# Performance work log

Measured on AMD Instinct MI355X. Metric: run time of the kernel, lower is better.

## Reference

```python
import jax, jax.numpy as jnp
import numpy as np

BS, DIM = 8192, 768
TEMPERATURE = 1.0
EPS = 1e-8


def setup_inputs() -> dict:
    key = jax.random.key(0)
    k1, k2 = jax.random.split(key)
    text_emb = jax.random.normal(k1, (BS, DIM), dtype=jnp.float32)
    ctr_emb = jax.random.normal(k2, (BS, DIM), dtype=jnp.float32)
    return {"text_emb": text_emb, "ctr_emb": ctr_emb}


def _l2norm(x):
    # cosine scorer normalization
    return x / jnp.maximum(jnp.linalg.norm(x, axis=-1, keepdims=True), EPS)


def reference(text_emb, ctr_emb):
    t = _l2norm(text_emb)          # [bs, d]
    c = _l2norm(ctr_emb)           # [bs, d]
    # S[i, j] = cos(text_i, ctr_j) / T  -- single GEMM instead of (bs,bs,d) broadcast
    S = jnp.einsum('id,jd->ij', t, c) / TEMPERATURE   # [bs, bs]
    sim_ii = jnp.diagonal(S)                           # [bs]
    # loss1_i = lse_j S[i,j] - S[i,i]; loss2_i = lse_j S[j,i] - S[i,i]
    loss = (jax.nn.logsumexp(S, axis=1)
            + jax.nn.logsumexp(S, axis=0)
            - 2.0 * sim_ii)
    return jnp.mean(loss)
```

## Files before the change

### kernel.cpp

```cpp
#include <hip/hip_runtime.h>
#include <hip/hip_bf16.h>

#define BS   8192
#define DIM  768
#define TILE 128
#define BK   128

typedef float f32x4 __attribute__((ext_vector_type(4)));
typedef int   i32x4 __attribute__((ext_vector_type(4)));
typedef int   i32x8 __attribute__((ext_vector_type(8)));

__device__ __forceinline__ void async16(const void* g, void* l) {
    __builtin_amdgcn_global_load_lds(
        (const __attribute__((address_space(1))) unsigned int*)g,
        (__attribute__((address_space(3))) unsigned int*)l,
        16, 0, 0);
}

__global__ __launch_bounds__(256) void normalize_kernel(
    const float* __restrict__ text, const float* __restrict__ ctr,
    unsigned char* __restrict__ tq, unsigned char* __restrict__ cq,
    float* __restrict__ sim) {
    const int lane = threadIdx.x & 63;
    const int row  = blockIdx.x * 4 + (threadIdx.x >> 6);
    const size_t base = (size_t)row * DIM;

    float4 t[3], c[3];
    float st = 0.f, sc = 0.f, sd = 0.f;
#pragma unroll
    for (int i = 0; i < 3; ++i) {
        t[i] = *(const float4*)&text[base + lane * 4 + i * 256];
        c[i] = *(const float4*)&ctr [base + lane * 4 + i * 256];
        st += t[i].x*t[i].x + t[i].y*t[i].y + t[i].z*t[i].z + t[i].w*t[i].w;
        sc += c[i].x*c[i].x + c[i].y*c[i].y + c[i].z*c[i].z + c[i].w*c[i].w;
        sd += t[i].x*c[i].x + t[i].y*c[i].y + t[i].z*c[i].z + t[i].w*c[i].w;
    }
#pragma unroll
    for (int off = 1; off < 64; off <<= 1) {
        st += __shfl_xor(st, off);
        sc += __shfl_xor(sc, off);
        sd += __shfl_xor(sd, off);
    }
    const float invt = 1.0f / fmaxf(sqrtf(st), 1e-8f);
    const float invc = 1.0f / fmaxf(sqrtf(sc), 1e-8f);
#pragma unroll
    for (int i = 0; i < 3; ++i) {
        unsigned int wt = (unsigned int)__builtin_amdgcn_cvt_pk_fp8_f32(t[i].x * invt, t[i].y * invt, 0, false);
        wt = (unsigned int)__builtin_amdgcn_cvt_pk_fp8_f32(t[i].z * invt, t[i].w * invt, (int)wt, true);
        unsigned int wcq = (unsigned int)__builtin_amdgcn_cvt_pk_fp8_f32(c[i].x * invc, c[i].y * invc, 0, false);
        wcq = (unsigned int)__builtin_amdgcn_cvt_pk_fp8_f32(c[i].z * invc, c[i].w * invc, (int)wcq, true);
        *(unsigned int*)&tq[base + lane * 4 + i * 256] = wt;
        *(unsigned int*)&cq[base + lane * 4 + i * 256] = wcq;
    }
    if (lane == 0) sim[row] = sd * invt * invc;
}

__global__ __launch_bounds__(256) void gemm_lse_kernel(
    const unsigned char* __restrict__ tq, const unsigned char* __restrict__ cq,
    float* __restrict__ rowsum, float* __restrict__ colsum) {
    __shared__ char ldsA[TILE * BK];
    __shared__ char ldsB[TILE * BK];

    const int tid = threadIdx.x;

    const int bid = blockIdx.x;
    const int xcd = bid & 7, idx = bid >> 3;
    const int tileCol = idx >> 3, rowInBand = idx & 7;
    const int rowBase = (xcd * 8 + rowInBand) * TILE;
    const int colBase = tileCol * TILE;

    const int wave = tid >> 6, lane = tid & 63;
    const int wr = wave >> 1, wc = wave & 1;
    const int quad = lane >> 4, l16 = lane & 15;

    int goff[4];
    char *dstA[4], *dstB[4];
#pragma unroll
    for (int i = 0; i < 4; ++i) {
        const int p  = tid + i * 256;
        const int kc = p >> 8;
        const int row = (p >> 1) & 127;
        const int hl  = (p & 1) ^ (kc & 1);
        goff[i] = row * DIM + kc * 32 + hl * 16;
        dstA[i] = ldsA + p * 16;
        dstB[i] = ldsB + p * 16;
    }
    const unsigned char* gA = tq + (size_t)rowBase * DIM;
    const unsigned char* gB = cq + (size_t)colBase * DIM;

    const int sw = quad & 1;
    int aoff[4], boff[4];
#pragma unroll
    for (int mt = 0; mt < 4; ++mt) aoff[mt] = quad * 4096 + (wr * 64 + mt * 16 + l16) * 32;
#pragma unroll
    for (int nt = 0; nt < 4; ++nt) boff[nt] = quad * 4096 + (wc * 64 + nt * 16 + l16) * 32;

    f32x4 acc[4][4];
#pragma unroll
    for (int mt = 0; mt < 4; ++mt)
#pragma unroll
        for (int nt = 0; nt < 4; ++nt)
            acc[mt][nt] = (f32x4){0.f, 0.f, 0.f, 0.f};

    for (int k0 = 0; k0 < DIM; k0 += BK) {
#pragma unroll
        for (int i = 0; i < 4; ++i) {
            async16(gA + goff[i] + k0, dstA[i]);
            async16(gB + goff[i] + k0, dstB[i]);
        }
        __syncthreads();

        i32x8 af[4], bf[4];
#pragma unroll
        for (int mt = 0; mt < 4; ++mt) {
            i32x4 lo = *(const i32x4*)(ldsA + aoff[mt] + sw * 16);
            i32x4 hi = *(const i32x4*)(ldsA + aoff[mt] + (sw ^ 1) * 16);
            af[mt] = __builtin_shufflevector(lo, hi, 0, 1, 2, 3, 4, 5, 6, 7);
        }
#pragma unroll
        for (int nt = 0; nt < 4; ++nt) {
            i32x4 lo = *(const i32x4*)(ldsB + boff[nt] + sw * 16);
            i32x4 hi = *(const i32x4*)(ldsB + boff[nt] + (sw ^ 1) * 16);
            bf[nt] = __builtin_shufflevector(lo, hi, 0, 1, 2, 3, 4, 5, 6, 7);
        }

#pragma unroll
        for (int mt = 0; mt < 4; ++mt)
#pragma unroll
            for (int nt = 0; nt < 4; ++nt)
                acc[mt][nt] = __builtin_amdgcn_mfma_scale_f32_16x16x128_f8f6f4(
                    af[mt], bf[nt], acc[mt][nt], 0, 0, 0, 127, 0, 127);
        __syncthreads();
    }

    float rp[4][4];
    float cp[4];
#pragma unroll
    for (int mt = 0; mt < 4; ++mt)
#pragma unroll
        for (int r = 0; r < 4; ++r) rp[mt][r] = 0.f;
#pragma unroll
    for (int nt = 0; nt < 4; ++nt) cp[nt] = 0.f;

#pragma unroll
    for (int mt = 0; mt < 4; ++mt)
#pragma unroll
        for (int nt = 0; nt < 4; ++nt)
#pragma unroll
            for (int r = 0; r < 4; ++r) {
                const float e = __expf(acc[mt][nt][r]);
                rp[mt][r] += e;
                cp[nt]    += e;
            }

#pragma unroll
    for (int mt = 0; mt < 4; ++mt)
#pragma unroll
        for (int r = 0; r < 4; ++r) {
            float v = rp[mt][r];
            v += __shfl_xor(v, 1);
            v += __shfl_xor(v, 2);
            v += __shfl_xor(v, 4);
            v += __shfl_xor(v, 8);
            rp[mt][r] = v;
        }
    if (l16 == 0) {
#pragma unroll
        for (int mt = 0; mt < 4; ++mt)
#pragma unroll
            for (int r = 0; r < 4; ++r)
                atomicAdd(&rowsum[rowBase + wr * 64 + mt * 16 + quad * 4 + r], rp[mt][r]);
    }
#pragma unroll
    for (int nt = 0; nt < 4; ++nt) {
        float v = cp[nt];
        v += __shfl_xor(v, 16);
        v += __shfl_xor(v, 32);
        if (quad == 0)
            atomicAdd(&colsum[colBase + wc * 64 + nt * 16 + l16], v);
    }
}

__global__ __launch_bounds__(256) void finalize_kernel(
    const float* __restrict__ rowsum, const float* __restrict__ colsum,
    const float* __restrict__ sim, float* __restrict__ out) {
    const int tid = threadIdx.x;
    float acc = 0.f;
    for (int i = tid; i < BS; i += 256)
        acc += logf(rowsum[i]) + logf(colsum[i]) - 2.f * sim[i];
#pragma unroll
    for (int off = 1; off < 64; off <<= 1) acc += __shfl_xor(acc, off);
    __shared__ float red[4];
    const int wave = tid >> 6, lane = tid & 63;
    if (lane == 0) red[wave] = acc;
    __syncthreads();
    if (tid == 0) out[0] = (red[0] + red[1] + red[2] + red[3]) / (float)BS;
}

extern "C" void kernel_launch(void* const* d_in, const int* in_sizes, int n_in,
                              void* d_out, int out_size, void* d_ws, size_t ws_size,
                              hipStream_t stream) {
    const float* text = (const float*)d_in[0];
    const float* ctr  = (const float*)d_in[1];

    char* ws = (char*)d_ws;
    const size_t embBytes = (size_t)BS * DIM;
    unsigned char* tq = (unsigned char*)ws;
    unsigned char* cq = (unsigned char*)(ws + embBytes);
    float* sim    = (float*)(ws + 2 * embBytes);
    float* rowsum = (float*)(ws + 2 * embBytes + BS * sizeof(float));
    float* colsum = (float*)(ws + 2 * embBytes + 2 * BS * sizeof(float));

    hipMemsetAsync(rowsum, 0, 2 * BS * sizeof(float), stream);

    normalize_kernel<<<BS / 4, 256, 0, stream>>>(text, ctr, tq, cq, sim);

    gemm_lse_kernel<<<(BS / TILE) * (BS / TILE), 256, 0, stream>>>(tq, cq, rowsum, colsum);

    finalize_kernel<<<1, 256, 0, stream>>>(rowsum, colsum, sim, (float*)d_out);
}
```

Baseline: 204.9 us.

## Use 256x256 tiles with double-buffered LDS and fuse finalize into GEMM

Result: slower. 263.5 us (+28.6%).

```diff
diff --git a/kernel.cpp b/kernel.cpp
--- a/kernel.cpp
+++ b/kernel.cpp
@@ -3,8 +3,11 @@
 
 #define BS   8192
 #define DIM  768
-#define TILE 128
+#define TM   256
+#define TN   256
 #define BK   128
+#define NIT  (DIM / BK)
+#define GRID ((BS / TM) * (BS / TN))
 
 typedef float f32x4 __attribute__((ext_vector_type(4)));
 typedef int   i32x4 __attribute__((ext_vector_type(4)));
@@ -20,7 +23,14 @@
 __global__ __launch_bounds__(256) void normalize_kernel(
     const float* __restrict__ text, const float* __restrict__ ctr,
     unsigned char* __restrict__ tq, unsigned char* __restrict__ cq,
-    float* __restrict__ sim) {
+    float* __restrict__ sim, float* __restrict__ rowsum, float* __restrict__ colsum,
+    unsigned int* __restrict__ cnt) {
+    if (blockIdx.x < 64) {
+        const int i = blockIdx.x * 256 + threadIdx.x;
+        rowsum[i] = 0.f;
+        colsum[i] = 0.f;
+    }
+    if (blockIdx.x == 64 && threadIdx.x == 0) *cnt = 0u;
     const int lane = threadIdx.x & 63;
     const int row  = blockIdx.x * 4 + (threadIdx.x >> 6);
     const size_t base = (size_t)row * DIM;
@@ -55,35 +65,33 @@
     if (lane == 0) sim[row] = sd * invt * invc;
 }
 
-__global__ __launch_bounds__(256) void gemm_lse_kernel(
+__global__ __launch_bounds__(1024) void gemm_lse_kernel(
     const unsigned char* __restrict__ tq, const unsigned char* __restrict__ cq,
-    float* __restrict__ rowsum, float* __restrict__ colsum) {
-    __shared__ char ldsA[TILE * BK];
-    __shared__ char ldsB[TILE * BK];
+    float* __restrict__ rowsum, float* __restrict__ colsum,
+    const float* __restrict__ sim, unsigned int* __restrict__ cnt,
+    float* __restrict__ out) {
+    __shared__ char lds[2 * 65536];
 
     const int tid = threadIdx.x;
 
     const int bid = blockIdx.x;
     const int xcd = bid & 7, idx = bid >> 3;
-    const int tileCol = idx >> 3, rowInBand = idx & 7;
-    const int rowBase = (xcd * 8 + rowInBand) * TILE;
-    const int colBase = tileCol * TILE;
+    const int rowBase = (xcd * 4 + (idx & 3)) * TM;
+    const int colBase = (idx >> 2) * TN;
 
     const int wave = tid >> 6, lane = tid & 63;
-    const int wr = wave >> 1, wc = wave & 1;
+    const int wr = wave >> 2, wc = wave & 3;
     const int quad = lane >> 4, l16 = lane & 15;
 
-    int goff[4];
-    char *dstA[4], *dstB[4];
-#pragma unroll
-    for (int i = 0; i < 4; ++i) {
-        const int p  = tid + i * 256;
-        const int kc = p >> 8;
-        const int row = (p >> 1) & 127;
+    int gofs[2], lofs[2];
+#pragma unroll
+    for (int i = 0; i < 2; ++i) {
+        const int p   = tid + i * 1024;
+        const int kc  = p >> 9;
+        const int row = (p >> 1) & 255;
         const int hl  = (p & 1) ^ (kc & 1);
-        goff[i] = row * DIM + kc * 32 + hl * 16;
-        dstA[i] = ldsA + p * 16;
-        dstB[i] = ldsB + p * 16;
+        gofs[i] = row * DIM + kc * 32 + hl * 16;
+        lofs[i] = p * 16;
     }
     const unsigned char* gA = tq + (size_t)rowBase * DIM;
     const unsigned char* gB = cq + (size_t)colBase * DIM;
@@ -91,9 +99,9 @@
     const int sw = quad & 1;
     int aoff[4], boff[4];
 #pragma unroll
-    for (int mt = 0; mt < 4; ++mt) aoff[mt] = quad * 4096 + (wr * 64 + mt * 16 + l16) * 32;
-#pragma unroll
-    for (int nt = 0; nt < 4; ++nt) boff[nt] = quad * 4096 + (wc * 64 + nt * 16 + l16) * 32;
+    for (int mt = 0; mt < 4; ++mt) aoff[mt] = quad * 8192 + (wr * 64 + mt * 16 + l16) * 32;
+#pragma unroll
+    for (int nt = 0; nt < 4; ++nt) boff[nt] = quad * 8192 + (wc * 64 + nt * 16 + l16) * 32;
 
     f32x4 acc[4][4];
 #pragma unroll
@@ -102,35 +110,43 @@
         for (int nt = 0; nt < 4; ++nt)
             acc[mt][nt] = (f32x4){0.f, 0.f, 0.f, 0.f};
 
-    for (int k0 = 0; k0 < DIM; k0 += BK) {
-#pragma unroll
-        for (int i = 0; i < 4; ++i) {
-            async16(gA + goff[i] + k0, dstA[i]);
-            async16(gB + goff[i] + k0, dstB[i]);
-        }
+#pragma unroll
+    for (int i = 0; i < 2; ++i) {
+        async16(gA + gofs[i], lds + lofs[i]);
+        async16(gB + gofs[i], lds + 32768 + lofs[i]);
+    }
+
+    for (int it = 0; it < NIT; ++it) {
         __syncthreads();
-
-        i32x8 af[4], bf[4];
+        if (it + 1 < NIT) {
+            const int k0 = (it + 1) * BK;
+            char* nb = lds + ((it + 1) & 1) * 65536;
+#pragma unroll
+            for (int i = 0; i < 2; ++i) {
+                async16(gA + gofs[i] + k0, nb + lofs[i]);
+                async16(gB + gofs[i] + k0, nb + 32768 + lofs[i]);
+            }
+        }
+        const char* bA = lds + (it & 1) * 65536;
+        const char* bB = bA + 32768;
+
+        i32x8 bfr[4];
+#pragma unroll
+        for (int nt = 0; nt < 4; ++nt) {
+            i32x4 lo = *(const i32x4*)(bB + boff[nt] + sw * 16);
+            i32x4 hi = *(const i32x4*)(bB + boff[nt] + (sw ^ 1) * 16);
+            bfr[nt] = __builtin_shufflevector(lo, hi, 0, 1, 2, 3, 4, 5, 6, 7);
+        }
 #pragma unroll
         for (int mt = 0; mt < 4; ++mt) {
-            i32x4 lo = *(const i32x4*)(ldsA + aoff[mt] + sw * 16);
-            i32x4 hi = *(const i32x4*)(ldsA + aoff[mt] + (sw ^ 1) * 16);
-            af[mt] = __builtin_shufflevector(lo, hi, 0, 1, 2, 3, 4, 5, 6, 7);
-        }
-#pragma unroll
-        for (int nt = 0; nt < 4; ++nt) {
-            i32x4 lo = *(const i32x4*)(ldsB + boff[nt] + sw * 16);
-            i32x4 hi = *(const i32x4*)(ldsB + boff[nt] + (sw ^ 1) * 16);
-            bf[nt] = __builtin_shufflevector(lo, hi, 0, 1, 2, 3, 4, 5, 6, 7);
-        }
-
-#pragma unroll
-        for (int mt = 0; mt < 4; ++mt)
+            i32x4 lo = *(const i32x4*)(bA + aoff[mt] + sw * 16);
+            i32x4 hi = *(const i32x4*)(bA + aoff[mt] + (sw ^ 1) * 16);
+            i32x8 af = __builtin_shufflevector(lo, hi, 0, 1, 2, 3, 4, 5, 6, 7);
 #pragma unroll
             for (int nt = 0; nt < 4; ++nt)
                 acc[mt][nt] = __builtin_amdgcn_mfma_scale_f32_16x16x128_f8f6f4(
-                    af[mt], bf[nt], acc[mt][nt], 0, 0, 0, 127, 0, 127);
-        __syncthreads();
+                    af, bfr[nt], acc[mt][nt], 0, 0, 0, 127, 0, 127);
+        }
     }
 
     float rp[4][4];
@@ -179,22 +195,36 @@
         if (quad == 0)
             atomicAdd(&colsum[colBase + wc * 64 + nt * 16 + l16], v);
     }
-}
-
-__global__ __launch_bounds__(256) void finalize_kernel(
-    const float* __restrict__ rowsum, const float* __restrict__ colsum,
-    const float* __restrict__ sim, float* __restrict__ out) {
-    const int tid = threadIdx.x;
-    float acc = 0.f;
-    for (int i = tid; i < BS; i += 256)
-        acc += logf(rowsum[i]) + logf(colsum[i]) - 2.f * sim[i];
-#pragma unroll
-    for (int off = 1; off < 64; off <<= 1) acc += __shfl_xor(acc, off);
-    __shared__ float red[4];
-    const int wave = tid >> 6, lane = tid & 63;
-    if (lane == 0) red[wave] = acc;
+
+    float* redf = (float*)lds;
+    unsigned int* flagp = (unsigned int*)(lds + 128);
     __syncthreads();
-    if (tid == 0) out[0] = (red[0] + red[1] + red[2] + red[3]) / (float)BS;
+    if (tid == 0) {
+        unsigned int old = __hip_atomic_fetch_add(cnt, 1u, __ATOMIC_ACQ_REL,
+                                                  __HIP_MEMORY_SCOPE_AGENT);
+        *flagp = (old == GRID - 1) ? 1u : 0u;
+    }
+    __syncthreads();
+    if (*flagp) {
+        float a = 0.f;
+        for (int j = tid; j < BS; j += 1024) {
+            const float rs = __hip_atomic_load(&rowsum[j], __ATOMIC_RELAXED,
+                                               __HIP_MEMORY_SCOPE_AGENT);
+            const float cs = __hip_atomic_load(&colsum[j], __ATOMIC_RELAXED,
+                                               __HIP_MEMORY_SCOPE_AGENT);
+            a += __logf(rs) + __logf(cs) - 2.f * sim[j];
+        }
+#pragma unroll
+        for (int off = 1; off < 64; off <<= 1) a += __shfl_xor(a, off);
+        if (lane == 0) redf[wave] = a;
+        __syncthreads();
+        if (tid == 0) {
+            float s = 0.f;
+#pragma unroll
+            for (int w = 0; w < 16; ++w) s += redf[w];
+            out[0] = s / (float)BS;
+        }
+    }
 }
 
 extern "C" void kernel_launch(void* const* d_in, const int* in_sizes, int n_in,
@@ -210,12 +240,11 @@
     float* sim    = (float*)(ws + 2 * embBytes);
     float* rowsum = (float*)(ws + 2 * embBytes + BS * sizeof(float));
     float* colsum = (float*)(ws + 2 * embBytes + 2 * BS * sizeof(float));
-
-    hipMemsetAsync(rowsum, 0, 2 * BS * sizeof(float), stream);
-
-    normalize_kernel<<<BS / 4, 256, 0, stream>>>(text, ctr, tq, cq, sim);
-
-    gemm_lse_kernel<<<(BS / TILE) * (BS / TILE), 256, 0, stream>>>(tq, cq, rowsum, colsum);
-
-    finalize_kernel<<<1, 256, 0, stream>>>(rowsum, colsum, sim, (float*)d_out);
-}
+    unsigned int* cnt = (unsigned int*)(ws + 2 * embBytes + 3 * BS * sizeof(float));
+
+    normalize_kernel<<<BS / 4, 256, 0, stream>>>(text, ctr, tq, cq, sim,
+                                                 rowsum, colsum, cnt);
+
+    gemm_lse_kernel<<<GRID, 1024, 0, stream>>>(tq, cq, rowsum, colsum, sim,
+                                               cnt, (float*)d_out);
+}
```
